# Performance work log

Hardware: AMD Instinct MI355X
Metric: run time of the kernel (lower is better)

Reference implementation:

```python
import jax, jax.numpy as jnp
import numpy as np

N_EMBD = 2048
N_HEAD = 16
HEAD_DIM = N_EMBD // N_HEAD
ROPE_THETA = 10000.0


def _rope_cache(seq_len, head_dim, theta):
    inv_freq = 1.0 / theta ** (jnp.arange(0, head_dim, 2, dtype=jnp.float32) / head_dim)
    t = jnp.arange(seq_len, dtype=jnp.float32)
    freqs = jnp.outer(t, inv_freq)  # [S, head_dim//2]
    return jnp.cos(freqs), jnp.sin(freqs)


def _apply_rope(x, cos, sin):
    # x: [B, H, S, D]; cos/sin: [S, D//2] -> broadcast over B, H
    cos = cos[None, None, :, :]
    sin = sin[None, None, :, :]
    x1 = x[..., ::2]
    x2 = x[..., 1::2]
    rot = jnp.stack((x1 * cos - x2 * sin, x1 * sin + x2 * cos), axis=-1)
    return rot.reshape(x.shape)


def setup_inputs() -> dict:
    key = jax.random.key(0)
    ks = jax.random.split(key, 5)
    scale = 1.0 / np.sqrt(N_EMBD)
    x = jax.random.normal(ks[0], (2, 2048, N_EMBD), dtype=jnp.float32)
    wq = jax.random.normal(ks[1], (N_EMBD, N_EMBD), dtype=jnp.float32) * scale
    wk = jax.random.normal(ks[2], (N_EMBD, N_EMBD), dtype=jnp.float32) * scale
    wv = jax.random.normal(ks[3], (N_EMBD, N_EMBD), dtype=jnp.float32) * scale
    wo = jax.random.normal(ks[4], (N_EMBD, N_EMBD), dtype=jnp.float32) * scale
    return {"x": x, "wq": wq, "wk": wk, "wv": wv, "wo": wo}


def reference(x, wq, wk, wv, wo):
    bsz, seq_len, _ = x.shape
    q = (x @ wq).reshape(bsz, seq_len, N_HEAD, HEAD_DIM).transpose(0, 2, 1, 3)
    k = (x @ wk).reshape(bsz, seq_len, N_HEAD, HEAD_DIM).transpose(0, 2, 1, 3)
    v = (x @ wv).reshape(bsz, seq_len, N_HEAD, HEAD_DIM).transpose(0, 2, 1, 3)

    cos, sin = _rope_cache(seq_len, HEAD_DIM, ROPE_THETA)
    q = _apply_rope(q, cos, sin)
    k = _apply_rope(k, cos, sin)

    scale = 1.0 / np.sqrt(HEAD_DIM)
    att = jnp.einsum('bhqd,bhkd->bhqk', q, k) * scale  # [B,H,S,S]
    causal = jnp.tril(jnp.ones((seq_len, seq_len), dtype=bool))
    att = jnp.where(causal[None, None, :, :], att, -jnp.inf)
    att = jax.nn.softmax(att, axis=-1)
    y = jnp.einsum('bhqk,bhkd->bhqd', att, v)  # [B,H,S,D]
    y = y.transpose(0, 2, 1, 3).reshape(bsz, seq_len, N_EMBD)
    return y @ wo
```

## Files before the change

kernel.cpp:

```cpp
#include <hip/hip_runtime.h>
#include <math.h>

constexpr int BSZ = 2;
constexpr int SEQ = 2048;
constexpr int NE  = 2048;
constexpr int NH  = 16;
constexpr int HD  = 128;
constexpr int MROWS = BSZ * SEQ;

typedef __bf16 bf16x8 __attribute__((ext_vector_type(8)));
typedef float  f32x4  __attribute__((ext_vector_type(4)));

__device__ __forceinline__ unsigned short f2bf(float f) {
    union { float f; unsigned u; } v; v.f = f;
    unsigned r = v.u + 0x7fffu + ((v.u >> 16) & 1u);
    return (unsigned short)(r >> 16);
}
__device__ __forceinline__ float bf2f(unsigned short s) {
    union { unsigned u; float f; } v; v.u = ((unsigned)s) << 16; return v.f;
}

__device__ __forceinline__ void load_lds16(const void* g, void* l) {
    __builtin_amdgcn_global_load_lds(
        (const __attribute__((address_space(1))) unsigned int*)g,
        (__attribute__((address_space(3))) unsigned int*)l, 16, 0, 0);
}

template <int CTRL>
__device__ __forceinline__ float dpp_mv(float x) {
    int v = __builtin_amdgcn_update_dpp(
        0, __builtin_bit_cast(int, x), CTRL, 0xF, 0xF, true);
    return __builtin_bit_cast(float, v);
}
__device__ __forceinline__ float row16_max(float x) {
    x = fmaxf(x, dpp_mv<0xB1>(x));
    x = fmaxf(x, dpp_mv<0x4E>(x));
    x = fmaxf(x, dpp_mv<0x124>(x));
    x = fmaxf(x, dpp_mv<0x128>(x));
    return x;
}
__device__ __forceinline__ float row16_sum(float x) {
    x += dpp_mv<0xB1>(x);
    x += dpp_mv<0x4E>(x);
    x += dpp_mv<0x124>(x);
    x += dpp_mv<0x128>(x);
    return x;
}

__global__ __launch_bounds__(256) void cast_f32_bf16(const float* __restrict__ in,
                                                     ushort* __restrict__ out, int n)
{
    int i = (blockIdx.x * 256 + threadIdx.x) * 4;
    if (i >= n) return;
    float4 v = *(const float4*)(in + i);
    ushort4 o;
    o.x = f2bf(v.x); o.y = f2bf(v.y); o.z = f2bf(v.z); o.w = f2bf(v.w);
    *(ushort4*)(out + i) = o;
}

__global__ __launch_bounds__(256) void transpose_cast(const float* __restrict__ w0,
                                                      const float* __restrict__ w1,
                                                      const float* __restrict__ w2,
                                                      const float* __restrict__ w3,
                                                      ushort* __restrict__ o0,
                                                      ushort* __restrict__ o1,
                                                      ushort* __restrict__ o2,
                                                      ushort* __restrict__ o3)
{
    const float* S; ushort* D;
    switch (blockIdx.z) {
        case 0: S = w0; D = o0; break;
        case 1: S = w1; D = o1; break;
        case 2: S = w2; D = o2; break;
        default: S = w3; D = o3; break;
    }
    __shared__ float t[32][33];
    const int tx = threadIdx.x, ty = threadIdx.y;
    const int x0 = blockIdx.x * 32, y0 = blockIdx.y * 32;
#pragma unroll
    for (int i = 0; i < 4; ++i)
        t[ty + i * 8][tx] = S[(size_t)(y0 + ty + i * 8) * NE + x0 + tx];
    __syncthreads();
#pragma unroll
    for (int i = 0; i < 4; ++i)
        D[(size_t)(x0 + ty + i * 8) * NE + y0 + tx] = f2bf(t[tx][ty + i * 8]);
}

__global__ __launch_bounds__(256) void gemm_qkv(const ushort* __restrict__ A,
                                                const ushort* __restrict__ W,
                                                ushort* __restrict__ Qb,
                                                ushort* __restrict__ Kb,
                                                ushort* __restrict__ Vt)
{
    __shared__ ushort Al[128 * 32];
    __shared__ ushort Bl[128 * 32];

    const int tid  = threadIdx.x;
    const int w    = tid >> 6;
    const int lane = tid & 63;
    const int quad = lane >> 4;
    const int r    = lane & 15;
    const int wm   = w & 1;
    const int wn   = w >> 1;
    const int m0 = blockIdx.y * 128;
    const int n0 = blockIdx.x * 128;
    const int K  = NE;

    const int arow0 = tid >> 2;           const int akp = (tid & 3) * 8;
    const int arow1 = (256 + tid) >> 2;

    f32x4 acc[4][4] = {};

    for (int k0 = 0; k0 < K; k0 += 32) {
        load_lds16(A + (size_t)(m0 + arow0) * K + k0 + akp, &Al[(size_t)w * 512]);
        load_lds16(A + (size_t)(m0 + arow1) * K + k0 + akp, &Al[(size_t)(4 + w) * 512]);
        load_lds16(W + (size_t)(n0 + arow0) * K + k0 + akp, &Bl[(size_t)w * 512]);
        load_lds16(W + (size_t)(n0 + arow1) * K + k0 + akp, &Bl[(size_t)(4 + w) * 512]);
        __syncthreads();

        bf16x8 af[4], bfr[4];
#pragma unroll
        for (int it = 0; it < 4; ++it)
            af[it] = *(const bf16x8*)&Al[(wm * 64 + it * 16 + r) * 32 + quad * 8];
#pragma unroll
        for (int jt = 0; jt < 4; ++jt)
            bfr[jt] = *(const bf16x8*)&Bl[(wn * 64 + jt * 16 + r) * 32 + quad * 8];
#pragma unroll
        for (int it = 0; it < 4; ++it)
#pragma unroll
            for (int jt = 0; jt < 4; ++jt)
                acc[it][jt] = __builtin_amdgcn_mfma_f32_16x16x32_bf16(
                    af[it], bfr[jt], acc[it][jt], 0, 0, 0);
        __syncthreads();
    }

    const int mat  = n0 >> 11;
    const int ncol = n0 & 2047;
    if (mat < 2) {
        ushort* C = mat ? Kb : Qb;
#pragma unroll
        for (int it = 0; it < 4; ++it) {
            const int row = m0 + wm * 64 + it * 16 + quad * 4;
#pragma unroll
            for (int jt = 0; jt < 4; ++jt) {
                const int col = ncol + wn * 64 + jt * 16 + r;
#pragma unroll
                for (int reg = 0; reg < 4; ++reg)
                    C[(size_t)(row + reg) * NE + col] = f2bf(acc[it][jt][reg]);
            }
        }
    } else {
#pragma unroll
        for (int it = 0; it < 4; ++it) {
            const int row = m0 + wm * 64 + it * 16 + quad * 4;
            const int bb = row >> 11;
            const int s  = row & 2047;
#pragma unroll
            for (int jt = 0; jt < 4; ++jt) {
                const int col = ncol + wn * 64 + jt * 16 + r;
                const int hh = col >> 7;
                const int d  = col & 127;
                ushort4 pk;
                pk.x = f2bf(acc[it][jt][0]); pk.y = f2bf(acc[it][jt][1]);
                pk.z = f2bf(acc[it][jt][2]); pk.w = f2bf(acc[it][jt][3]);
                *(ushort4*)&Vt[((size_t)((bb * NH + hh) * HD + d)) * SEQ + s] = pk;
            }
        }
    }
}

__global__ __launch_bounds__(256) void gemm_out(const ushort* __restrict__ A,
                                                const ushort* __restrict__ Bt,
                                                float* __restrict__ C)
{
    __shared__ ushort Al[128 * 32];
    __shared__ ushort Bl[128 * 32];

    const int tid  = threadIdx.x;
    const int w    = tid >> 6;
    const int lane = tid & 63;
    const int quad = lane >> 4;
    const int r    = lane & 15;
    const int wm   = w & 1;
    const int wn   = w >> 1;
    const int m0 = blockIdx.y * 128;
    const int n0 = blockIdx.x * 128;
    const int K  = NE;

    const int arow0 = tid >> 2;           const int akp = (tid & 3) * 8;
    const int arow1 = (256 + tid) >> 2;

    f32x4 acc[4][4] = {};

    for (int k0 = 0; k0 < K; k0 += 32) {
        load_lds16(A  + (size_t)(m0 + arow0) * K + k0 + akp, &Al[(size_t)w * 512]);
        load_lds16(A  + (size_t)(m0 + arow1) * K + k0 + akp, &Al[(size_t)(4 + w) * 512]);
        load_lds16(Bt + (size_t)(n0 + arow0) * K + k0 + akp, &Bl[(size_t)w * 512]);
        load_lds16(Bt + (size_t)(n0 + arow1) * K + k0 + akp, &Bl[(size_t)(4 + w) * 512]);
        __syncthreads();

        bf16x8 af[4], bfr[4];
#pragma unroll
        for (int it = 0; it < 4; ++it)
            af[it] = *(const bf16x8*)&Al[(wm * 64 + it * 16 + r) * 32 + quad * 8];
#pragma unroll
        for (int jt = 0; jt < 4; ++jt)
            bfr[jt] = *(const bf16x8*)&Bl[(wn * 64 + jt * 16 + r) * 32 + quad * 8];
#pragma unroll
        for (int it = 0; it < 4; ++it)
#pragma unroll
            for (int jt = 0; jt < 4; ++jt)
                acc[it][jt] = __builtin_amdgcn_mfma_f32_16x16x32_bf16(
                    af[it], bfr[jt], acc[it][jt], 0, 0, 0);
        __syncthreads();
    }

#pragma unroll
    for (int it = 0; it < 4; ++it) {
        const int row = m0 + wm * 64 + it * 16 + quad * 4;
#pragma unroll
        for (int jt = 0; jt < 4; ++jt) {
            const int col = n0 + wn * 64 + jt * 16 + r;
#pragma unroll
            for (int reg = 0; reg < 4; ++reg)
                C[(size_t)(row + reg) * NE + col] = acc[it][jt][reg];
        }
    }
}

__global__ __launch_bounds__(256) void rope_bf16(ushort* __restrict__ Q,
                                                 ushort* __restrict__ K)
{
    const size_t npairs = (size_t)MROWS * NE / 2;
    size_t idx = (size_t)blockIdx.x * blockDim.x + threadIdx.x;
    if (idx >= npairs) return;
    ushort* P = blockIdx.y ? K : Q;

    const int r = (int)(idx / (NE / 2));
    const int c = (int)(idx % (NE / 2));
    const int s = r % SEQ;
    const int i = c & 63;

    const float inv_freq = exp2f((float)i * -0.20762050593046014f);
    const float f = (float)s * inv_freq;
    float sn, cs;
    sincosf(f, &sn, &cs);

    unsigned* p = (unsigned*)(P + (size_t)r * NE) + c;
    unsigned v = *p;
    const float x1 = bf2f((unsigned short)(v & 0xffffu));
    const float x2 = bf2f((unsigned short)(v >> 16));
    const float y1 = x1 * cs - x2 * sn;
    const float y2 = x1 * sn + x2 * cs;
    *p = (unsigned)f2bf(y1) | ((unsigned)f2bf(y2) << 16);
}

__global__ __launch_bounds__(256, 2) void flash_attn(const ushort* __restrict__ Qg,
                                                     const ushort* __restrict__ Kg,
                                                     const ushort* __restrict__ Vtg,
                                                     ushort* __restrict__ Yg)
{
    const int qt = (int)gridDim.x - 1 - (int)blockIdx.x;
    const int bh = blockIdx.y;
    const int b = bh >> 4, h = bh & 15;
    const int tid  = threadIdx.x;
    const int w    = tid >> 6;
    const int lane = tid & 63;
    const int quad = lane >> 4;
    const int r    = lane & 15;

    __shared__ ushort Ks[64][136];
    __shared__ ushort Vts[128][72];
    __shared__ ushort Ps[64][72];

    const int q0 = qt * 64;
    const size_t qkbase = (size_t)b * SEQ * NE + (size_t)h * HD;
    const size_t vbase  = (size_t)(bh * HD) * SEQ;
    const float scale = 0.088388347648318447f;

    bf16x8 aq[4];
    {
        const ushort* qrow = Qg + qkbase + (size_t)(q0 + w * 16 + r) * NE;
#pragma unroll
        for (int kc = 0; kc < 4; ++kc)
            aq[kc] = *(const bf16x8*)(qrow + kc * 32 + quad * 8);
    }

    float m_i[4], l_i[4];
    f32x4 acc_o[8];
#pragma unroll
    for (int reg = 0; reg < 4; ++reg) { m_i[reg] = -INFINITY; l_i[reg] = 0.f; }
#pragma unroll
    for (int dt = 0; dt < 8; ++dt) acc_o[dt] = f32x4{0.f, 0.f, 0.f, 0.f};

    for (int t = 0; t <= qt; ++t) {
        const int j0 = t * 64;

        {
            const int row0 = tid >> 4;
            const int ch   = (tid & 15) * 8;
#pragma unroll
            for (int i = 0; i < 4; ++i) {
                const int row = i * 16 + row0;
                *(uint4*)&Ks[row][ch] =
                    *(const uint4*)(Kg + qkbase + (size_t)(j0 + row) * NE + ch);
            }
            const int d0  = tid >> 3;
            const int ch2 = (tid & 7) * 8;
#pragma unroll
            for (int i = 0; i < 4; ++i) {
                const int d = i * 32 + d0;
                *(uint4*)&Vts[d][ch2] =
                    *(const uint4*)(Vtg + vbase + (size_t)d * SEQ + j0 + ch2);
            }
        }
        __syncthreads();

        f32x4 sa[4];
#pragma unroll
        for (int jt = 0; jt < 4; ++jt) {
            f32x4 acc = {0.f, 0.f, 0.f, 0.f};
#pragma unroll
            for (int kc = 0; kc < 4; ++kc) {
                bf16x8 bk = *(const bf16x8*)&Ks[jt * 16 + r][kc * 32 + quad * 8];
                acc = __builtin_amdgcn_mfma_f32_16x16x32_bf16(aq[kc], bk, acc, 0, 0, 0);
            }
            sa[jt] = acc;
        }

        if (t == qt) {
#pragma unroll
            for (int jt = 0; jt < 4; ++jt)
#pragma unroll
                for (int reg = 0; reg < 4; ++reg)
                    sa[jt][reg] = (jt * 16 + r > w * 16 + quad * 4 + reg)
                                  ? -INFINITY : sa[jt][reg] * scale;
        } else {
#pragma unroll
            for (int jt = 0; jt < 4; ++jt)
#pragma unroll
                for (int reg = 0; reg < 4; ++reg)
                    sa[jt][reg] *= scale;
        }

        float rmax[4], alpha[4], rsum[4];
#pragma unroll
        for (int reg = 0; reg < 4; ++reg) {
            rmax[reg] = fmaxf(fmaxf(sa[0][reg], sa[1][reg]),
                              fmaxf(sa[2][reg], sa[3][reg]));
            rmax[reg] = row16_max(rmax[reg]);
        }

#pragma unroll
        for (int reg = 0; reg < 4; ++reg) {
            const float mnew = fmaxf(m_i[reg], rmax[reg]);
            alpha[reg] = __expf(m_i[reg] - mnew);
            m_i[reg] = mnew;
            rsum[reg] = 0.f;
        }
#pragma unroll
        for (int jt = 0; jt < 4; ++jt)
#pragma unroll
            for (int reg = 0; reg < 4; ++reg) {
                const float p = __expf(sa[jt][reg] - m_i[reg]);
                sa[jt][reg] = p;
                rsum[reg] += p;
            }
#pragma unroll
        for (int reg = 0; reg < 4; ++reg) {
            rsum[reg] = row16_sum(rsum[reg]);
            l_i[reg] = l_i[reg] * alpha[reg] + rsum[reg];
        }

#pragma unroll
        for (int jt = 0; jt < 4; ++jt)
#pragma unroll
            for (int reg = 0; reg < 4; ++reg)
                Ps[w * 16 + quad * 4 + reg][jt * 16 + r] = f2bf(sa[jt][reg]);

#pragma unroll
        for (int dt = 0; dt < 8; ++dt)
#pragma unroll
            for (int reg = 0; reg < 4; ++reg)
                acc_o[dt][reg] *= alpha[reg];

        bf16x8 ap[2];
#pragma unroll
        for (int kc = 0; kc < 2; ++kc)
            ap[kc] = *(const bf16x8*)&Ps[w * 16 + r][kc * 32 + quad * 8];
#pragma unroll
        for (int dt = 0; dt < 8; ++dt)
#pragma unroll
            for (int kc = 0; kc < 2; ++kc) {
                bf16x8 bv = *(const bf16x8*)&Vts[dt * 16 + r][kc * 32 + quad * 8];
                acc_o[dt] = __builtin_amdgcn_mfma_f32_16x16x32_bf16(ap[kc], bv, acc_o[dt], 0, 0, 0);
            }
        __syncthreads();
    }

#pragma unroll
    for (int reg = 0; reg < 4; ++reg) {
        const float inv = 1.0f / l_i[reg];
        const size_t rowbase = qkbase + (size_t)(q0 + w * 16 + quad * 4 + reg) * NE;
#pragma unroll
        for (int dt = 0; dt < 8; ++dt)
            Yg[rowbase + dt * 16 + r] = f2bf(acc_o[dt][reg] * inv);
    }
}

extern "C" void kernel_launch(void* const* d_in, const int* in_sizes, int n_in,
                              void* d_out, int out_size, void* d_ws, size_t ws_size,
                              hipStream_t stream)
{
    const float* x  = (const float*)d_in[0];
    const float* wq = (const float*)d_in[1];
    const float* wk = (const float*)d_in[2];
    const float* wv = (const float*)d_in[3];
    const float* wo = (const float*)d_in[4];
    float* out = (float*)d_out;

    ushort* ws = (ushort*)d_ws;
    const size_t MAT  = (size_t)MROWS * NE;
    const size_t WMAT = (size_t)NE * NE;
    ushort* xb  = ws;
    ushort* wqT = xb + MAT;
    ushort* wkT = wqT + WMAT;
    ushort* wvT = wkT + WMAT;
    ushort* woT = wvT + WMAT;
    ushort* Qb  = woT + WMAT;
    ushort* Kb  = Qb + MAT;
    ushort* Vt  = Kb + MAT;
    ushort* Yb  = Qb;

    cast_f32_bf16<<<(unsigned)(MAT / 4 / 256), 256, 0, stream>>>(x, xb, (int)MAT);
    transpose_cast<<<dim3(64, 64, 4), dim3(32, 8), 0, stream>>>(
        wq, wk, wv, wo, wqT, wkT, wvT, woT);

    gemm_qkv<<<dim3(48, 32), 256, 0, stream>>>(xb, wqT, Qb, Kb, Vt);

    const size_t npairs = (size_t)MROWS * NE / 2;
    rope_bf16<<<dim3((unsigned)(npairs / 256), 2), 256, 0, stream>>>(Qb, Kb);

    flash_attn<<<dim3(SEQ / 64, BSZ * NH), 256, 0, stream>>>(Qb, Kb, Vt, Yb);

    gemm_out<<<dim3(16, 32), 256, 0, stream>>>(Yb, woT, out);
}
```

Measured before the change: 501.4 us.

## Fuse RoPE into QKV GEMM epilogue, merge cast kernels, swizzle GEMM tiles

Applies RoPE inside the QKV GEMM epilogue. Adjacent column pairs are exchanged with a DPP lane swap, which removes the separate rope kernel and its read-modify-write pass over Q and K. The x cast is folded into the weight transpose/cast launch as an extra grid slice, saving one launch. Both GEMMs also remap block indices with a swizzle to improve L2 reuse of A/B tiles. The trade-off is that sincos is now computed per output element in the GEMM epilogue, adding work there.

```diff
diff --git a/kernel.cpp b/kernel.cpp
--- a/kernel.cpp
+++ b/kernel.cpp
@@ -47,26 +47,30 @@
     return x;
 }
 
-__global__ __launch_bounds__(256) void cast_f32_bf16(const float* __restrict__ in,
-                                                     ushort* __restrict__ out, int n)
-{
-    int i = (blockIdx.x * 256 + threadIdx.x) * 4;
-    if (i >= n) return;
-    float4 v = *(const float4*)(in + i);
-    ushort4 o;
-    o.x = f2bf(v.x); o.y = f2bf(v.y); o.z = f2bf(v.z); o.w = f2bf(v.w);
-    *(ushort4*)(out + i) = o;
-}
-
-__global__ __launch_bounds__(256) void transpose_cast(const float* __restrict__ w0,
+__global__ __launch_bounds__(256) void transpose_cast(const float* __restrict__ xf,
+                                                      const float* __restrict__ w0,
                                                       const float* __restrict__ w1,
                                                       const float* __restrict__ w2,
                                                       const float* __restrict__ w3,
+                                                      ushort* __restrict__ xb,
                                                       ushort* __restrict__ o0,
                                                       ushort* __restrict__ o1,
                                                       ushort* __restrict__ o2,
                                                       ushort* __restrict__ o3)
 {
+    if (blockIdx.z == 4) {
+        const int tid = threadIdx.y * 32 + threadIdx.x;
+        const size_t i = (((size_t)blockIdx.y * 64 + blockIdx.x) * 256 + tid) * 8;
+        float4 v0 = *(const float4*)(xf + i);
+        float4 v1 = *(const float4*)(xf + i + 4);
+        ushort4 a, b;
+        a.x = f2bf(v0.x); a.y = f2bf(v0.y); a.z = f2bf(v0.z); a.w = f2bf(v0.w);
+        b.x = f2bf(v1.x); b.y = f2bf(v1.y); b.z = f2bf(v1.z); b.w = f2bf(v1.w);
+        *(ushort4*)(xb + i)     = a;
+        *(ushort4*)(xb + i + 4) = b;
+        return;
+    }
+
     const float* S; ushort* D;
     switch (blockIdx.z) {
         case 0: S = w0; D = o0; break;
@@ -102,8 +106,10 @@
     const int r    = lane & 15;
     const int wm   = w & 1;
     const int wn   = w >> 1;
-    const int m0 = blockIdx.y * 128;
-    const int n0 = blockIdx.x * 128;
+    const int lin = (int)blockIdx.y * 48 + (int)blockIdx.x;
+    const int swz = (lin & 7) * 192 + (lin >> 3);
+    const int m0 = (swz / 48) * 128;
+    const int n0 = (swz % 48) * 128;
     const int K  = NE;
 
     const int arow0 = tid >> 2;           const int akp = (tid & 3) * 8;
@@ -138,6 +144,13 @@
     const int ncol = n0 & 2047;
     if (mat < 2) {
         ushort* C = mat ? Kb : Qb;
+        float invf[4];
+#pragma unroll
+        for (int jt = 0; jt < 4; ++jt) {
+            const int d = (wn * 64 + jt * 16 + r) & 127;
+            invf[jt] = exp2f((float)(d >> 1) * -0.20762050593046014f);
+        }
+        const float sgn = (r & 1) ? 1.0f : -1.0f;
 #pragma unroll
         for (int it = 0; it < 4; ++it) {
             const int row = m0 + wm * 64 + it * 16 + quad * 4;
@@ -145,8 +158,15 @@
             for (int jt = 0; jt < 4; ++jt) {
                 const int col = ncol + wn * 64 + jt * 16 + r;
 #pragma unroll
-                for (int reg = 0; reg < 4; ++reg)
-                    C[(size_t)(row + reg) * NE + col] = f2bf(acc[it][jt][reg]);
+                for (int reg = 0; reg < 4; ++reg) {
+                    const float self = acc[it][jt][reg];
+                    const float part = dpp_mv<0xB1>(self);
+                    const int s = (row + reg) & 2047;
+                    float sn, cs;
+                    sincosf((float)s * invf[jt], &sn, &cs);
+                    const float y = self * cs + sgn * part * sn;
+                    C[(size_t)(row + reg) * NE + col] = f2bf(y);
+                }
             }
         }
     } else {
@@ -183,8 +203,10 @@
     const int r    = lane & 15;
     const int wm   = w & 1;
     const int wn   = w >> 1;
-    const int m0 = blockIdx.y * 128;
-    const int n0 = blockIdx.x * 128;
+    const int lin = (int)blockIdx.y * 16 + (int)blockIdx.x;
+    const int swz = (lin & 7) * 64 + (lin >> 3);
+    const int m0 = (swz / 16) * 128;
+    const int n0 = (swz % 16) * 128;
     const int K  = NE;
 
     const int arow0 = tid >> 2;           const int akp = (tid & 3) * 8;
@@ -226,33 +248,6 @@
                 C[(size_t)(row + reg) * NE + col] = acc[it][jt][reg];
         }
     }
-}
-
-__global__ __launch_bounds__(256) void rope_bf16(ushort* __restrict__ Q,
-                                                 ushort* __restrict__ K)
-{
-    const size_t npairs = (size_t)MROWS * NE / 2;
-    size_t idx = (size_t)blockIdx.x * blockDim.x + threadIdx.x;
-    if (idx >= npairs) return;
-    ushort* P = blockIdx.y ? K : Q;
-
-    const int r = (int)(idx / (NE / 2));
-    const int c = (int)(idx % (NE / 2));
-    const int s = r % SEQ;
-    const int i = c & 63;
-
-    const float inv_freq = exp2f((float)i * -0.20762050593046014f);
-    const float f = (float)s * inv_freq;
-    float sn, cs;
-    sincosf(f, &sn, &cs);
-
-    unsigned* p = (unsigned*)(P + (size_t)r * NE) + c;
-    unsigned v = *p;
-    const float x1 = bf2f((unsigned short)(v & 0xffffu));
-    const float x2 = bf2f((unsigned short)(v >> 16));
-    const float y1 = x1 * cs - x2 * sn;
-    const float y2 = x1 * sn + x2 * cs;
-    *p = (unsigned)f2bf(y1) | ((unsigned)f2bf(y2) << 16);
 }
 
 __global__ __launch_bounds__(256, 2) void flash_attn(const ushort* __restrict__ Qg,
@@ -432,15 +427,11 @@
     ushort* Vt  = Kb + MAT;
     ushort* Yb  = Qb;
 
-    cast_f32_bf16<<<(unsigned)(MAT / 4 / 256), 256, 0, stream>>>(x, xb, (int)MAT);
-    transpose_cast<<<dim3(64, 64, 4), dim3(32, 8), 0, stream>>>(
-        wq, wk, wv, wo, wqT, wkT, wvT, woT);
+    transpose_cast<<<dim3(64, 64, 5), dim3(32, 8), 0, stream>>>(
+        x, wq, wk, wv, wo, xb, wqT, wkT, wvT, woT);
 
     gemm_qkv<<<dim3(48, 32), 256, 0, stream>>>(xb, wqT, Qb, Kb, Vt);
 
-    const size_t npairs = (size_t)MROWS * NE / 2;
-    rope_bf16<<<dim3((unsigned)(npairs / 256), 2), 256, 0, stream>>>(Qb, Kb);
-
     flash_attn<<<dim3(SEQ / 64, BSZ * NH), 256, 0, stream>>>(Qb, Kb, Vt, Yb);
 
     gemm_out<<<dim3(16, 32), 256, 0, stream>>>(Yb, woT, out);
```

Result: slower. 1.823 ms (+263.5%).
